# Optimization experiments

Hardware: AMD Instinct MI355X
Metric: run time of the kernel (lower is better)

## Reference

```python
import jax, jax.numpy as jnp
import numpy as np

N, E, EALL, C, R = 20000, 120000, 240000, 150, 1000
EH, RH, CH = 300, 100, 150


def _seg_softmax(e, idx, n):
    m = jax.ops.segment_max(e, idx, num_segments=n)
    ex = jnp.exp(e - m[idx])
    s = jax.ops.segment_sum(ex, idx, num_segments=n)
    return ex / s[idx]


def _l2norm(x):
    return x / jnp.clip(jnp.linalg.norm(x, axis=-1, keepdims=True), 1e-12, None)


def _highway(x1, x2, w, b):
    g = jax.nn.sigmoid(x1 @ w.T + b)
    return g * x2 + (1.0 - g) * x1


def _gcn(x, ei):
    n = x.shape[0]
    j, i = ei[0], ei[1]
    deg = jax.ops.segment_sum(jnp.ones(ei.shape[1], dtype=x.dtype), i, num_segments=n)
    dis = jnp.where(deg > 0, deg ** -0.5, 0.0)
    norm = dis[j] * dis[i]
    return jax.nn.relu(jax.ops.segment_sum(norm[:, None] * x[j], i, num_segments=n))


def _gat(x, ei, ai, aj):
    n = x.shape[0]
    j, i = ei[0], ei[1]
    e = (x @ ai)[i] + (x @ aj)[j]
    alpha = _seg_softmax(jax.nn.leaky_relu(e), i, n)
    return jax.nn.relu(jax.ops.segment_sum(alpha[:, None] * x[j], i, num_segments=n))


def _gat_e(x_e, im, io, rel, triple_num, r_emb, class_index, cls_ent,
           ac, ar, wh, wt, hww, hwb, main_is_head):
    n = x_e.shape[0]
    e_cnt = im.shape[0]
    c = cls_ent.shape[0]
    x_h = jax.nn.relu(x_e @ wh.T)
    x_t = jax.nn.relu(x_e @ wt.T)
    if main_is_head:
        x_m, x_o = x_h, x_t
        v1m, v2m, v3m = ac[0], ac[1], ac[2]
        v1o, v2o, v3o = ac[4], ac[5], ac[6]
    else:
        x_m, x_o = x_t, x_h
        v1m, v2m, v3m = ac[4], ac[5], ac[6]
        v1o, v2o, v3o = ac[0], ac[1], ac[2]
    v4, acv = ac[3], ac[7]
    e1 = 0.5 * ((x_m @ v1m)[im] + (x_o @ v1o)[io]) + (r_emb @ ar[0])[rel]
    alpha = _seg_softmax(jax.nn.leaky_relu(e1), triple_num, e_cnt)
    x_edge = _l2norm(x_m[im] * alpha[:, None])  # [E, c_hidden]
    e_r = 0.5 * ((r_emb @ ar[1])[rel] + 0.5 * ((x_edge @ v3m) + (x_o @ v3o)[io]))
    e = (x_o @ v2o)[io] + e_r + (x_edge @ v2m)
    beta = _seg_softmax(jax.nn.leaky_relu(e), class_index, c)
    # literal to source: the edge-level tensor is re-indexed by node ids in spmm
    x_class = jax.ops.segment_sum(beta[:, None] * x_edge[im], class_index, num_segments=c)
    e_c = (x_class @ acv) + (x_o @ v4)[cls_ent]
    gama = _seg_softmax(jax.nn.leaky_relu(e_c), cls_ent, n)
    out = jax.ops.segment_sum(gama[:, None] * x_class, cls_ent, num_segments=n)
    return _highway(x_o, out, hww, hwb)


def _forward(x_e, r_emb_table, hw1_w, hw1_b, hw2_w, hw2_b,
             h2r_ac, h2r_ar, h2r_wh, h2r_wt, h2r_hw_w, h2r_hw_b,
             et_ac, et_ar, et_wh, et_wt, et_hw_w, et_hw_b,
             gat_ai, gat_aj,
             edge_index, rel, edge_index_all, triple_num,
             class_index_head, head_class, class_index_tail, tail_class):
    r_emb = _l2norm(r_emb_table)
    x = _highway(x_e, _gcn(x_e, edge_index_all), hw1_w, hw1_b)
    x = _highway(x, _gcn(x, edge_index_all), hw2_w, hw2_b)
    eh, et = edge_index[0], edge_index[1]
    x_e_h = _gat_e(x, et, eh, rel, triple_num, r_emb, class_index_head, head_class,
                   h2r_ac, h2r_ar, h2r_wh, h2r_wt, h2r_hw_w, h2r_hw_b, False)
    x_e_t = _gat_e(x, eh, et, rel, triple_num, r_emb, class_index_tail, tail_class,
                   et_ac, et_ar, et_wh, et_wt, et_hw_w, et_hw_b, True)
    x1 = jnp.concatenate([x, x_e_h, x_e_t], axis=1)  # [N, 600]
    return jnp.concatenate([x, _gat(x1, edge_index_all, gat_ai, gat_aj)], axis=1)  # [N, 900]


def setup_inputs() -> dict:
    key = jax.random.key(0)
    ks = jax.random.split(key, 32)
    w = lambda k, shape: (jax.random.normal(k, shape, dtype=jnp.float32) * 0.05)
    return {
        'x_e': jax.random.normal(ks[0], (N, EH), dtype=jnp.float32),
        'edge_index': jax.random.randint(ks[1], (2, E), 0, N),
        'rel': jax.random.randint(ks[2], (E,), 0, R),
        'edge_index_all': jax.random.randint(ks[3], (2, EALL), 0, N),
        'triple_num': jax.random.randint(ks[4], (E,), 0, N),
        'class_index_head': jax.random.randint(ks[5], (E,), 0, C),
        'head_class': jax.random.randint(ks[6], (C,), 0, N),
        'class_index_tail': jax.random.randint(ks[7], (E,), 0, C),
        'tail_class': jax.random.randint(ks[8], (C,), 0, N),
        'r_emb_table': jax.random.normal(ks[9], (R, RH), dtype=jnp.float32),
        'hw1_w': w(ks[10], (EH, EH)), 'hw1_b': jnp.zeros((EH,), jnp.float32),
        'hw2_w': w(ks[11], (EH, EH)), 'hw2_b': jnp.zeros((EH,), jnp.float32),
        'h2r_ac': w(ks[12], (8, CH)), 'h2r_ar': w(ks[13], (2, RH)),
        'h2r_wh': w(ks[14], (CH, EH)), 'h2r_wt': w(ks[15], (CH, EH)),
        'h2r_hw_w': w(ks[16], (CH, CH)), 'h2r_hw_b': jnp.zeros((CH,), jnp.float32),
        'et_ac': w(ks[17], (8, CH)), 'et_ar': w(ks[18], (2, RH)),
        'et_wh': w(ks[19], (CH, EH)), 'et_wt': w(ks[20], (CH, EH)),
        'et_hw_w': w(ks[21], (CH, CH)), 'et_hw_b': jnp.zeros((CH,), jnp.float32),
        'gat_ai': w(ks[22], (2 * EH,)), 'gat_aj': w(ks[23], (2 * EH,)),
    }


def reference(x_e, edge_index, rel, edge_index_all, triple_num,
              class_index_head, head_class, class_index_tail, tail_class,
              r_emb_table, hw1_w, hw1_b, hw2_w, hw2_b,
              h2r_ac, h2r_ar, h2r_wh, h2r_wt, h2r_hw_w, h2r_hw_b,
              et_ac, et_ar, et_wh, et_wt, et_hw_w, et_hw_b,
              gat_ai, gat_aj):
    return _forward(x_e, r_emb_table, hw1_w, hw1_b, hw2_w, hw2_b,
                    h2r_ac, h2r_ar, h2r_wh, h2r_wt, h2r_hw_w, h2r_hw_b,
                    et_ac, et_ar, et_wh, et_wt, et_hw_w, et_hw_b,
                    gat_ai, gat_aj,
                    edge_index, rel, edge_index_all, triple_num,
                    class_index_head, head_class, class_index_tail, tail_class)
```

## Files before the change

kernel.cpp:

```cpp
#include <hip/hip_runtime.h>
#include <math.h>

#define Nn 20000
#define Ee 120000
#define EALLe 240000
#define Cc 150
#define Rr 1000
#define EHd 300
#define RHd 100
#define CHd 150
#define CB 128
#define XSPL 16

static inline int cdiv_h(int a, int b){ return (a + b - 1) / b; }

typedef __attribute__((ext_vector_type(8))) short short8;
typedef __attribute__((ext_vector_type(4))) float f32x4;

__device__ __forceinline__ float lrelu01(float x){ return x > 0.f ? x : 0.01f * x; }

__device__ __forceinline__ unsigned short f2b(float f){
  unsigned int u = __float_as_uint(f);
  unsigned int r = (u + 0x7FFFu + ((u >> 16) & 1u)) >> 16;
  return (unsigned short)r;
}
__device__ __forceinline__ float b2f(unsigned short u){
  return __uint_as_float(((unsigned int)u) << 16);
}
__device__ __forceinline__ float b2f_lo(unsigned int u){
  return __uint_as_float(u << 16);
}
__device__ __forceinline__ float b2f_hi(unsigned int u){
  return __uint_as_float(u & 0xFFFF0000u);
}

template<int Kq>
__device__ __forceinline__ void wredsumN(float* v){
#pragma unroll
  for (int m = 32; m >= 1; m >>= 1){
#pragma unroll
    for (int k = 0; k < Kq; k++) v[k] += __shfl_xor(v[k], m, 64);
  }
}

__global__ __launch_bounds__(64) void k_f2b(const float* __restrict__ src, int ncols,
    int ldsrc, unsigned short* __restrict__ dst, int ldp){
  int r = blockIdx.x, t = threadIdx.x;
  for (int c = t; c < ldp; c += 64)
    dst[(size_t)r * ldp + c] = (c < ncols) ? f2b(src[(size_t)r * ldsrc + c]) : (unsigned short)0;
}

__global__ __launch_bounds__(64) void k_f2bxo(const float* __restrict__ proj,
    unsigned short* __restrict__ xob){
  int r = blockIdx.x, g = blockIdx.y, t = threadIdx.x;
  const float* src = proj + (size_t)r * 600 + (g ? 450 : 0);
  unsigned short* dst = xob + (size_t)g * Nn * 160 + (size_t)r * 160;
  for (int c = t; c < 160; c += 64)
    dst[c] = (c < 150) ? f2b(src[c]) : (unsigned short)0;
}

__global__ __launch_bounds__(64) void k_rnorm(const float* __restrict__ rt,
    const float* __restrict__ arh, const float* __restrict__ are,
    float* __restrict__ ra1h, float* __restrict__ ra1e){
  int r = blockIdx.x, lane = threadIdx.x;
  bool m1 = (lane + 64 < RHd);
  float v0 = rt[r * RHd + lane];
  float v1 = m1 ? rt[r * RHd + lane + 64] : 0.f;
  float s[3];
  s[0] = v0 * v0 + v1 * v1;
  s[1] = v0 * arh[RHd + lane] + (m1 ? v1 * arh[RHd + lane + 64] : 0.f);
  s[2] = v0 * are[RHd + lane] + (m1 ? v1 * are[RHd + lane + 64] : 0.f);
  wredsumN<3>(s);
  float inv = 0.5f / fmaxf(sqrtf(s[0]), 1e-12f);
  if (!lane){
    ra1h[r] = s[1] * inv;
    ra1e[r] = s[2] * inv;
  }
}

__global__ void k_count(const int* __restrict__ dst, int* __restrict__ degi){
  int e = blockIdx.x * blockDim.x + threadIdx.x;
  if (e < EALLe) atomicAdd(&degi[dst[e]], 1);
}

__global__ void k_dis(const int* __restrict__ degi, float* __restrict__ dis){
  int n = blockIdx.x * blockDim.x + threadIdx.x;
  if (n < Nn) dis[n] = degi[n] > 0 ? rsqrtf((float)degi[n]) : 0.f;
}

__global__ __launch_bounds__(1024) void k_scan(const int* __restrict__ degi,
    int* __restrict__ ptr, int* __restrict__ cur){
  __shared__ int s[1024];
  int t = threadIdx.x;
  const int per = (Nn + 1023) / 1024;
  int b0 = t * per; if (b0 > Nn) b0 = Nn;
  int b1 = b0 + per; if (b1 > Nn) b1 = Nn;
  int sum = 0;
  for (int i = b0; i < b1; i++) sum += degi[i];
  s[t] = sum;
  __syncthreads();
  for (int off = 1; off < 1024; off <<= 1){
    int v = (t >= off) ? s[t - off] : 0;
    __syncthreads();
    s[t] += v;
    __syncthreads();
  }
  int run = (t > 0) ? s[t - 1] : 0;
  for (int i = b0; i < b1; i++){
    ptr[i] = run; cur[i] = run; run += degi[i];
  }
  if (t == 1023) ptr[Nn] = s[1023];
}

__global__ void k_scatter(const int* __restrict__ src, const int* __restrict__ dst,
    int* __restrict__ cur, int* __restrict__ csr_src){
  int e = blockIdx.x * blockDim.x + threadIdx.x;
  if (e >= EALLe) return;
  int pos = atomicAdd(&cur[dst[e]], 1);
  csr_src[pos] = src[e];
}

__global__ __launch_bounds__(64) void k_gcnb(const unsigned short* __restrict__ x, int ldx,
    const int* __restrict__ ptr, const int* __restrict__ src,
    const float* __restrict__ dis, float* __restrict__ out){
  int i = blockIdx.x, lane = threadIdx.x;
  int p0 = ptr[i], p1 = ptr[i + 1];
  float di = dis[i];
  float a0 = 0.f, a1 = 0.f, a2 = 0.f, a3 = 0.f, a4 = 0.f;
  for (int k = p0; k < p1; k++){
    int j = src[k];
    float w = di * dis[j];
    const unsigned short* xr = x + (size_t)j * ldx;
    a0 += w * b2f(xr[lane]);
    a1 += w * b2f(xr[lane + 64]);
    a2 += w * b2f(xr[lane + 128]);
    a3 += w * b2f(xr[lane + 192]);
    if (lane < EHd - 256) a4 += w * b2f(xr[lane + 256]);
  }
  float* orow = out + (size_t)i * EHd;
  orow[lane] = fmaxf(a0, 0.f);
  orow[lane + 64] = fmaxf(a1, 0.f);
  orow[lane + 128] = fmaxf(a2, 0.f);
  orow[lane + 192] = fmaxf(a3, 0.f);
  if (lane < EHd - 256) orow[lane + 256] = fmaxf(a4, 0.f);
}

__global__ __launch_bounds__(256) void k_gat3(const float* __restrict__ x1,
    const unsigned short* __restrict__ x1b,
    const int* __restrict__ ptr, const int* __restrict__ src,
    const float* __restrict__ s1, const float* __restrict__ s2,
    float* __restrict__ dout){
  __shared__ float wl[128];
  __shared__ int jl[128];
  int i = blockIdx.x, t = threadIdx.x;
  float* orow = dout + (size_t)i * 900;
  const float* xi = x1 + (size_t)i * 600;
  if (t < 75) ((f32x4*)orow)[t] = ((const f32x4*)xi)[t];
  int p0 = ptr[i], p1 = ptr[i + 1];
  if (p0 == p1){
    for (int f = t; f < 600; f += 256) orow[300 + f] = 0.f;
    return;
  }
  float s1i = s1[i];
  bool m2 = t < 44;
  float a0 = 0.f, a1 = 0.f, c0 = 0.f, c1 = 0.f, den = 0.f;
  for (int base = p0; base < p1; base += 128){
    int k = base + t;
    if (t < 128 && k < p1){
      int j = src[k];
      jl[t] = j;
      wl[t] = expf(lrelu01(s1i + s2[j]));
    }
    __syncthreads();
    int lim = p1 - base; if (lim > 128) lim = 128;
    for (int q = 0; q < lim; q++){
      float w = wl[q];
      den += w;
      const unsigned short* xj = x1b + (size_t)jl[q] * 600;
      unsigned int u = *(const unsigned int*)&xj[2 * t];
      a0 += w * b2f_lo(u);
      a1 += w * b2f_hi(u);
      if (m2){
        unsigned int v = *(const unsigned int*)&xj[512 + 2 * t];
        c0 += w * b2f_lo(v);
        c1 += w * b2f_hi(v);
      }
    }
    __syncthreads();
  }
  float invd = 1.f / den;
  orow[300 + 2 * t] = fmaxf(a0 * invd, 0.f);
  orow[300 + 2 * t + 1] = fmaxf(a1 * invd, 0.f);
  if (m2){
    orow[300 + 512 + 2 * t] = fmaxf(c0 * invd, 0.f);
    orow[300 + 512 + 2 * t + 1] = fmaxf(c1 * invd, 0.f);
  }
}

template<int EPI, int MIR>
__global__ __launch_bounds__(256) void k_gemmb(
    const unsigned short* __restrict__ Xb, int ldxb, int nrows,
    const unsigned short* __restrict__ Wb, int Kp, int M,
    const float* __restrict__ bias,
    const float* __restrict__ X2, int ldx2,
    const float* __restrict__ Xf, int ldxf,
    float* __restrict__ out, int ldo,
    unsigned short* __restrict__ mir, int ldmir){
  __shared__ unsigned short Xs[64][40];
  __shared__ unsigned short Ws[64][40];
  int t = threadIdx.x;
  int wv = t >> 6, lane = t & 63;
  int c0 = blockIdx.x * 64, r0 = blockIdx.y * 64;
  int srow = t >> 2, skoff = (t & 3) * 8;
  int gxr = r0 + srow, gwr = c0 + srow;
  f32x4 acc[4] = {};
  for (int k0 = 0; k0 < Kp; k0 += 32){
    short8 xv = {0,0,0,0,0,0,0,0};
    short8 wv8 = {0,0,0,0,0,0,0,0};
    if (gxr < nrows) xv = *(const short8*)&Xb[(size_t)gxr * ldxb + k0 + skoff];
    if (gwr < M)     wv8 = *(const short8*)&Wb[(size_t)gwr * Kp + k0 + skoff];
    __syncthreads();
    *(short8*)&Xs[srow][skoff] = xv;
    *(short8*)&Ws[srow][skoff] = wv8;
    __syncthreads();
    int arow = wv * 16 + (lane & 15);
    int kk = (lane >> 4) * 8;
    short8 af = *(const short8*)&Xs[arow][kk];
#pragma unroll
    for (int j = 0; j < 4; j++){
      short8 bf = *(const short8*)&Ws[j * 16 + (lane & 15)][kk];
      acc[j] = __builtin_amdgcn_mfma_f32_16x16x32_bf16(af, bf, acc[j], 0, 0, 0);
    }
  }
  int rbase = r0 + wv * 16 + (lane >> 4) * 4;
  int cbase = c0 + (lane & 15);
#pragma unroll
  for (int j = 0; j < 4; j++){
    int c = cbase + j * 16;
    if (c >= M) continue;
#pragma unroll
    for (int r = 0; r < 4; r++){
      int row = rbase + r;
      if (row >= nrows) continue;
      float v = acc[j][r];
      float o;
      if (EPI == 0){
        o = fmaxf(v, 0.f);
      } else {
        float g = 1.f / (1.f + expf(-(v + bias[c])));
        o = g * X2[(size_t)row * ldx2 + c] + (1.f - g) * Xf[(size_t)row * ldxf + c];
      }
      out[(size_t)row * ldo + c] = o;
      if (MIR) mir[(size_t)row * ldmir + c] = f2b(o);
    }
  }
}

__global__ __launch_bounds__(256) void k_hwgemm(
    const unsigned short* __restrict__ xob,
    const unsigned short* __restrict__ hwwbA, const unsigned short* __restrict__ hwwbB,
    const float* __restrict__ hwbA, const float* __restrict__ hwbB,
    const float* __restrict__ outb, const float* __restrict__ proj,
    float* __restrict__ x1, unsigned short* __restrict__ x1b){
  __shared__ unsigned short Xs[64][40];
  __shared__ unsigned short Ws[64][40];
  int g = blockIdx.z;
  const unsigned short* Xb = xob + (size_t)g * Nn * 160;
  const unsigned short* Wb = g ? hwwbB : hwwbA;
  const float* bias = g ? hwbB : hwbA;
  const float* X2 = outb + (size_t)g * Nn * CHd;
  const float* Xf = proj + (g ? 450 : 0);
  float* outp = x1 + (g ? 450 : 300);
  unsigned short* mir = x1b + (g ? 450 : 300);
  int t = threadIdx.x;
  int wv = t >> 6, lane = t & 63;
  int c0 = blockIdx.x * 64, r0 = blockIdx.y * 64;
  int srow = t >> 2, skoff = (t & 3) * 8;
  int gxr = r0 + srow, gwr = c0 + srow;
  f32x4 acc[4] = {};
  for (int k0 = 0; k0 < 160; k0 += 32){
    short8 xv = {0,0,0,0,0,0,0,0};
    short8 wv8 = {0,0,0,0,0,0,0,0};
    if (gxr < Nn) xv = *(const short8*)&Xb[(size_t)gxr * 160 + k0 + skoff];
    if (gwr < 150) wv8 = *(const short8*)&Wb[(size_t)gwr * 160 + k0 + skoff];
    __syncthreads();
    *(short8*)&Xs[srow][skoff] = xv;
    *(short8*)&Ws[srow][skoff] = wv8;
    __syncthreads();
    int arow = wv * 16 + (lane & 15);
    int kk = (lane >> 4) * 8;
    short8 af = *(const short8*)&Xs[arow][kk];
#pragma unroll
    for (int j = 0; j < 4; j++){
      short8 bf = *(const short8*)&Ws[j * 16 + (lane & 15)][kk];
      acc[j] = __builtin_amdgcn_mfma_f32_16x16x32_bf16(af, bf, acc[j], 0, 0, 0);
    }
  }
  int rbase = r0 + wv * 16 + (lane >> 4) * 4;
  int cbase = c0 + (lane & 15);
#pragma unroll
  for (int j = 0; j < 4; j++){
    int c = cbase + j * 16;
    if (c >= 150) continue;
#pragma unroll
    for (int r = 0; r < 4; r++){
      int row = rbase + r;
      if (row >= Nn) continue;
      float v = acc[j][r];
      float gg = 1.f / (1.f + expf(-(v + bias[c])));
      float o = gg * X2[(size_t)row * CHd + c] + (1.f - gg) * Xf[(size_t)row * 600 + c];
      outp[(size_t)row * 600 + c] = o;
      mir[(size_t)row * 600 + c] = f2b(o);
    }
  }
}

__global__ __launch_bounds__(64) void k_ndots2b(const float* __restrict__ proj,
    const float* __restrict__ h2r_ac, const float* __restrict__ et_ac,
    unsigned short* __restrict__ xnb, float* __restrict__ pm,
    float* __restrict__ po, float* __restrict__ nv4){
  int n = blockIdx.x, g = blockIdx.y, lane = threadIdx.x;
  const float* ac = g ? et_ac : h2r_ac;
  const float* xm = proj + (g ? 300 : 150);
  const float* xo = proj + (g ? 450 : 0);
  const float* v2m = ac + (g ? 1 : 5) * CHd;
  const float* v2o = ac + (g ? 5 : 1) * CHd;
  const float* v3m = ac + (g ? 2 : 6) * CHd;
  const float* v3o = ac + (g ? 6 : 2) * CHd;
  const float* v4  = ac + 3 * CHd;
  bool m2 = lane < (CHd - 128);
  const float* mr = xm + (size_t)n * 600;
  const float* orw = xo + (size_t)n * 600;
  float m0 = mr[lane], m1 = mr[lane + 64], mv2 = m2 ? mr[lane + 128] : 0.f;
  float o0 = orw[lane], o1 = orw[lane + 64], o2 = m2 ? orw[lane + 128] : 0.f;
  float s[4];
  s[0] = m0 * m0 + m1 * m1 + mv2 * mv2;
  s[1] = o0 * v2o[lane] + o1 * v2o[lane + 64] + (m2 ? o2 * v2o[lane + 128] : 0.f);
  s[2] = o0 * v3o[lane] + o1 * v3o[lane + 64] + (m2 ? o2 * v3o[lane + 128] : 0.f);
  s[3] = o0 * v4[lane]  + o1 * v4[lane + 64]  + (m2 ? o2 * v4[lane + 128]  : 0.f);
  wredsumN<4>(s);
  float inv = 1.f / fmaxf(sqrtf(s[0]), 1e-12f);
  float n0 = m0 * inv, n1 = m1 * inv, n2 = mv2 * inv;
  unsigned short* xr = xnb + (size_t)g * Nn * 152 + (size_t)n * 152;
  xr[lane] = f2b(n0); xr[lane + 64] = f2b(n1);
  if (m2) xr[lane + 128] = f2b(n2);
  float d[2];
  d[0] = n0 * v2m[lane] + n1 * v2m[lane + 64] + (m2 ? n2 * v2m[lane + 128] : 0.f);
  d[1] = n0 * v3m[lane] + n1 * v3m[lane + 64] + (m2 ? n2 * v3m[lane + 128] : 0.f);
  wredsumN<2>(d);
  if (!lane){
    pm[g * Nn + n] = d[0] + 0.25f * d[1];
    po[g * Nn + n] = s[1] + 0.25f * s[2];
    nv4[g * Nn + n] = s[3];
  }
}

__global__ __launch_bounds__(256) void k_e2sumb(const int* __restrict__ ei,
    const int* __restrict__ rel, const int* __restrict__ cih, const int* __restrict__ cit,
    const float* __restrict__ pm, const float* __restrict__ po,
    const float* __restrict__ ra1h, const float* __restrict__ ra1e,
    float* __restrict__ es2, float* __restrict__ csum_p, int* __restrict__ ccnt_p){
  __shared__ float ls[Cc];
  __shared__ int lc[Cc];
  int t = threadIdx.x, g = blockIdx.y;
  const int* im = ei + (g ? 0 : Ee);
  const int* io = ei + (g ? Ee : 0);
  const int* ci = g ? cit : cih;
  const float* ra1 = g ? ra1e : ra1h;
  const float* pmg = pm + g * Nn;
  const float* pog = po + g * Nn;
  float* es2g = es2 + (size_t)g * Ee;
  float* csg = csum_p + g * Cc * 16;
  int* ccg = ccnt_p + g * Cc * 16;
  for (int c = t; c < Cc; c += 256){ ls[c] = 0.f; lc[c] = 0; }
  __syncthreads();
  for (int e = blockIdx.x * 256 + t; e < Ee; e += gridDim.x * 256){
    float v = lrelu01(pog[io[e]] + pmg[im[e]] + ra1[rel[e]]);
    float s = expf(v);
    es2g[e] = s;
    int c = ci[e];
    atomicAdd(&ls[c], s);
    atomicAdd(&lc[c], 1);
  }
  __syncthreads();
  for (int c = t; c < Cc; c += 256){
    if (lc[c]){
      atomicAdd(&csg[c * 16], ls[c]);
      atomicAdd(&ccg[c * 16], lc[c]);
    }
  }
}

__global__ __launch_bounds__(256) void k_cscanb(const int* __restrict__ ccnt_p,
    int* __restrict__ cstart, int* __restrict__ ccur_p){
  __shared__ int s[Cc + 1];
  int t = threadIdx.x, g = blockIdx.x;
  const int* ccg = ccnt_p + g * Cc * 16;
  int* csg = cstart + g * (Cc + 1);
  int* cug = ccur_p + g * Cc * 16;
  if (t == 0){
    int run = 0;
    for (int c = 0; c < Cc; c++){ s[c] = run; run += ccg[c * 16]; }
    s[Cc] = run;
  }
  __syncthreads();
  if (t <= Cc) csg[t] = s[t];
  if (t < Cc) cug[t * 16] = s[t];
}

__global__ __launch_bounds__(256) void k_cscatterb(const int* __restrict__ ei,
    const int* __restrict__ cih, const int* __restrict__ cit,
    const float* __restrict__ es2,
    int* __restrict__ ccur_p, int* __restrict__ crows, float* __restrict__ cw){
  __shared__ int lcnt[Cc];
  __shared__ int lbase[Cc];
  int t = threadIdx.x, g = blockIdx.y;
  const int* im = ei + (g ? 0 : Ee);
  const int* ci = g ? cit : cih;
  const float* es2g = es2 + (size_t)g * Ee;
  int* cug = ccur_p + g * Cc * 16;
  int* crg = crows + (size_t)g * Ee;
  float* cwg = cw + (size_t)g * Ee;
  int epb = (Ee + gridDim.x - 1) / gridDim.x;
  int e0 = blockIdx.x * epb, e1 = e0 + epb; if (e1 > Ee) e1 = Ee;
  for (int c = t; c < Cc; c += 256) lcnt[c] = 0;
  __syncthreads();
  int myr[4], myc[4], mye[4]; int cnt = 0;
  for (int e = e0 + t; e < e1; e += 256){
    int c = ci[e];
    myr[cnt] = atomicAdd(&lcnt[c], 1);
    myc[cnt] = c; mye[cnt] = e; cnt++;
  }
  __syncthreads();
  for (int c = t; c < Cc; c += 256)
    lbase[c] = lcnt[c] ? atomicAdd(&cug[c * 16], lcnt[c]) : 0;
  __syncthreads();
  for (int q = 0; q < cnt; q++){
    int pos = lbase[myc[q]] + myr[q];
    int e = mye[q];
    crg[pos] = im[im[e]];
    cwg[pos] = es2g[e];
  }
}

__global__ __launch_bounds__(192) void k_xclassBb(
    const int* __restrict__ cstart, const int* __restrict__ crows,
    const float* __restrict__ cw, const float* __restrict__ csum_p,
    const unsigned short* __restrict__ xnb, float* __restrict__ x_class){
  int g = blockIdx.y;
  int c = blockIdx.x / XSPL, sp = blockIdx.x % XSPL;
  int t = threadIdx.x;
  const int* csg = cstart + g * (Cc + 1);
  const int* crg = crows + (size_t)g * Ee;
  const float* cwg = cw + (size_t)g * Ee;
  const unsigned short* xng = xnb + (size_t)g * Nn * 152;
  float* xcg = x_class + g * Cc * CHd;
  int p0 = csg[c], p1 = csg[c + 1];
  int len = p1 - p0;
  if (len <= 0) return;
  int chunk = (len + XSPL - 1) / XSPL;
  int q0 = p0 + sp * chunk;
  int q1 = q0 + chunk; if (q1 > p1) q1 = p1;
  if (q0 >= q1) return;
  bool act = t < CHd;
  float inv = 1.f / csum_p[g * Cc * 16 + c * 16];
  float acc = 0.f;
  int k = q0;
  for (; k + 4 <= q1; k += 4){
    int r0 = crg[k], r1 = crg[k + 1], r2 = crg[k + 2], r3 = crg[k + 3];
    float w0 = cwg[k] * inv, w1 = cwg[k + 1] * inv, w2 = cwg[k + 2] * inv, w3 = cwg[k + 3] * inv;
    if (act){
      acc += w0 * b2f(xng[(size_t)r0 * 152 + t]) + w1 * b2f(xng[(size_t)r1 * 152 + t])
           + w2 * b2f(xng[(size_t)r2 * 152 + t]) + w3 * b2f(xng[(size_t)r3 * 152 + t]);
    }
  }
  for (; k < q1; k++){
    if (act) acc += cwg[k] * inv * b2f(xng[(size_t)crg[k] * 152 + t]);
  }
  if (act) atomicAdd(&xcg[c * CHd + t], acc);
}

__global__ __launch_bounds__(256) void k_classfinalb(
    const float* __restrict__ x_class,
    const float* __restrict__ h2r_ac, const float* __restrict__ et_ac,
    const float* __restrict__ nv4,
    const int* __restrict__ hcls, const int* __restrict__ tcls,
    float* __restrict__ outb){
  __shared__ float v[Cc];
  __shared__ float gm[Cc];
  __shared__ int ce[Cc];
  int t = threadIdx.x, g = blockIdx.x;
  const float* xcg = x_class + g * Cc * CHd;
  const float* acv = (g ? et_ac : h2r_ac) + 7 * CHd;
  const float* nvg = nv4 + g * Nn;
  const int* cls_ent = g ? tcls : hcls;
  float* obg = outb + (size_t)g * Nn * CHd;
  if (t < Cc){
    ce[t] = cls_ent[t];
    float dot = 0.f;
    for (int f = 0; f < CHd; f++) dot += xcg[t * CHd + f] * acv[f];
    v[t] = lrelu01(dot + nvg[ce[t]]);
  }
  __syncthreads();
  if (t < Cc){
    int sgm = ce[t];
    float m = -3.0e38f;
    for (int c2 = 0; c2 < Cc; c2++) if (ce[c2] == sgm) m = fmaxf(m, v[c2]);
    float sum = 0.f;
    for (int c2 = 0; c2 < Cc; c2++) if (ce[c2] == sgm) sum += expf(v[c2] - m);
    gm[t] = expf(v[t] - m) / sum;
  }
  __syncthreads();
  for (int idx = t; idx < Cc * CHd; idx += 256){
    int c = idx / CHd, f = idx - c * CHd;
    atomicAdd(&obg[(size_t)ce[c] * CHd + f], gm[c] * xcg[c * CHd + f]);
  }
}

__global__ __launch_bounds__(64) void k_s12(const unsigned short* __restrict__ x1b,
    const float* __restrict__ ai, const float* __restrict__ aj,
    float* __restrict__ s1, float* __restrict__ s2){
  int n = blockIdx.x, lane = threadIdx.x;
  const unsigned short* xr = x1b + (size_t)n * 600;
  float sa = 0.f, sb = 0.f;
#pragma unroll
  for (int u = 0; u < 10; u++){
    int f = lane + u * 64;
    if (f < 600){
      float x = b2f(xr[f]);
      sa += x * ai[f];
      sb += x * aj[f];
    }
  }
  float s[2] = { sa, sb };
  wredsumN<2>(s);
  if (!lane){ s1[n] = s[0]; s2[n] = s[1]; }
}

extern "C" void kernel_launch(void* const* d_in, const int* in_sizes, int n_in,
                              void* d_out, int out_size, void* d_ws, size_t ws_size,
                              hipStream_t stream) {
  const float* x_e    = (const float*)d_in[0];
  const int*   ei     = (const int*)d_in[1];
  const int*   rel    = (const int*)d_in[2];
  const int*   eall   = (const int*)d_in[3];
  const int*   cih    = (const int*)d_in[5];
  const int*   hcls   = (const int*)d_in[6];
  const int*   cit    = (const int*)d_in[7];
  const int*   tcls   = (const int*)d_in[8];
  const float* remb   = (const float*)d_in[9];
  const float* hw1w   = (const float*)d_in[10];
  const float* hw1b   = (const float*)d_in[11];
  const float* hw2w   = (const float*)d_in[12];
  const float* hw2b   = (const float*)d_in[13];
  const float* h2r_ac = (const float*)d_in[14];
  const float* h2r_ar = (const float*)d_in[15];
  const float* h2r_wh = (const float*)d_in[16];
  const float* h2r_wt = (const float*)d_in[17];
  const float* h2r_hww= (const float*)d_in[18];
  const float* h2r_hwb= (const float*)d_in[19];
  const float* et_ac  = (const float*)d_in[20];
  const float* et_ar  = (const float*)d_in[21];
  const float* et_wh  = (const float*)d_in[22];
  const float* et_wt  = (const float*)d_in[23];
  const float* et_hww = (const float*)d_in[24];
  const float* et_hwb = (const float*)d_in[25];
  const float* gai    = (const float*)d_in[26];
  const float* gaj    = (const float*)d_in[27];
  float* out = (float*)d_out;

  char* wsp = (char*)d_ws;
  auto alloc = [&](size_t nbytes) -> void* {
    void* p = (void*)wsp;
    wsp += (nbytes + 255) & ~(size_t)255;
    return p;
  };
  float* ra1h = (float*)alloc(Rr * 4);
  float* ra1e = (float*)alloc(Rr * 4);
  float* dis  = (float*)alloc(Nn * 4);
  int* degi    = (int*)alloc(Nn * 4);
  int* csr_ptr = (int*)alloc((Nn + 1) * 4);
  int* csr_cur = (int*)alloc(Nn * 4);
  int* csr_src = (int*)alloc((size_t)EALLe * 4);
  float* x1  = (float*)alloc((size_t)Nn * 600 * 4);
  float* es2 = (float*)alloc((size_t)2 * Ee * 4);
  float* pm  = (float*)alloc(2 * Nn * 4);
  float* po  = (float*)alloc(2 * Nn * 4);
  float* nv4 = (float*)alloc(2 * Nn * 4);
  float* csum_p = (float*)alloc(2 * Cc * 16 * 4);
  int*   ccnt_p = (int*)alloc(2 * Cc * 16 * 4);
  float* x_class = (float*)alloc(2 * Cc * CHd * 4);
  size_t zregion = (size_t)((char*)x_class + ((2 * Cc * CHd * 4 + 255) & ~255)) - (size_t)(char*)csum_p;
  int*   ccur_p = (int*)alloc(2 * Cc * 16 * 4);
  int*   cstart = (int*)alloc(2 * (Cc + 1) * 4);
  int*   crows  = (int*)alloc((size_t)2 * Ee * 4);
  float* cw     = (float*)alloc((size_t)2 * Ee * 4);
  float* s1v = (float*)alloc(Nn * 4);
  float* s2v = (float*)alloc(Nn * 4);
  unsigned short* arenaA = (unsigned short*)alloc((size_t)Nn * 320 * 2);
  unsigned short* arenaB = (unsigned short*)alloc((size_t)Nn * 320 * 2);
  unsigned short* x1b    = (unsigned short*)alloc(((size_t)Nn * 600 + 64) * 2);
  unsigned short* w1b    = (unsigned short*)alloc((size_t)300 * 320 * 2);
  unsigned short* w2b    = (unsigned short*)alloc((size_t)300 * 320 * 2);
  unsigned short* wcatb  = (unsigned short*)alloc((size_t)600 * 320 * 2);
  unsigned short* hwwbA  = (unsigned short*)alloc((size_t)150 * 160 * 2);
  unsigned short* hwwbB  = (unsigned short*)alloc((size_t)150 * 160 * 2);
  unsigned short* xob = arenaA;
  unsigned short* xnb = arenaB;

  float* h1   = out;
  float* gbuf = out + (size_t)Nn * EHd;
  float* proj = out;
  float* outb = out + (size_t)Nn * 600;

  hipMemsetAsync(degi, 0, Nn * 4, stream);
  hipMemsetAsync(csum_p, 0, zregion, stream);
  hipMemsetAsync(outb, 0, (size_t)2 * Nn * CHd * 4, stream);
  k_rnorm<<<Rr, 64, 0, stream>>>(remb, h2r_ar, et_ar, ra1h, ra1e);
  k_count<<<cdiv_h(EALLe, 256), 256, 0, stream>>>(eall + EALLe, degi);
  k_dis<<<cdiv_h(Nn, 256), 256, 0, stream>>>(degi, dis);
  k_scan<<<1, 1024, 0, stream>>>(degi, csr_ptr, csr_cur);
  k_scatter<<<cdiv_h(EALLe, 256), 256, 0, stream>>>(eall, eall + EALLe, csr_cur, csr_src);
  k_f2b<<<300, 64, 0, stream>>>(hw1w, 300, 300, w1b, 320);
  k_f2b<<<300, 64, 0, stream>>>(hw2w, 300, 300, w2b, 320);
  k_f2b<<<150, 64, 0, stream>>>(h2r_wh, 300, 300, wcatb + (size_t)0   * 320, 320);
  k_f2b<<<150, 64, 0, stream>>>(h2r_wt, 300, 300, wcatb + (size_t)150 * 320, 320);
  k_f2b<<<150, 64, 0, stream>>>(et_wh,  300, 300, wcatb + (size_t)300 * 320, 320);
  k_f2b<<<150, 64, 0, stream>>>(et_wt,  300, 300, wcatb + (size_t)450 * 320, 320);
  k_f2b<<<150, 64, 0, stream>>>(h2r_hww, 150, 150, hwwbA, 160);
  k_f2b<<<150, 64, 0, stream>>>(et_hww,  150, 150, hwwbB, 160);
  k_f2b<<<Nn, 64, 0, stream>>>(x_e, 300, 300, arenaA, 320);

  k_gcnb<<<Nn, 64, 0, stream>>>(arenaA, 320, csr_ptr, csr_src, dis, gbuf);
  k_gemmb<1,1><<<dim3(5, cdiv_h(Nn, 64)), 256, 0, stream>>>(
      arenaA, 320, Nn, w1b, 320, 300, hw1b, gbuf, 300, x_e, 300, h1, 300, arenaB, 320);
  k_gcnb<<<Nn, 64, 0, stream>>>(arenaB, 320, csr_ptr, csr_src, dis, gbuf);
  k_gemmb<1,1><<<dim3(5, cdiv_h(Nn, 64)), 256, 0, stream>>>(
      arenaB, 320, Nn, w2b, 320, 300, hw2b, gbuf, 300, h1, 300, x1, 600, x1b, 600);

  k_gemmb<0,0><<<dim3(10, cdiv_h(Nn, 64)), 256, 0, stream>>>(
      x1b, 600, Nn, wcatb, 320, 600, nullptr, nullptr, 0, nullptr, 0, proj, 600,
      nullptr, 0);

  k_f2bxo<<<dim3(Nn, 2), 64, 0, stream>>>(proj, xob);
  k_ndots2b<<<dim3(Nn, 2), 64, 0, stream>>>(proj, h2r_ac, et_ac, xnb, pm, po, nv4);
  k_e2sumb<<<dim3(CB, 2), 256, 0, stream>>>(ei, rel, cih, cit, pm, po, ra1h, ra1e,
                                            es2, csum_p, ccnt_p);
  k_cscanb<<<2, 256, 0, stream>>>(ccnt_p, cstart, ccur_p);
  k_cscatterb<<<dim3(CB, 2), 256, 0, stream>>>(ei, cih, cit, es2, ccur_p, crows, cw);
  k_xclassBb<<<dim3(Cc * XSPL, 2), 192, 0, stream>>>(cstart, crows, cw, csum_p,
                                                     xnb, x_class);
  k_classfinalb<<<2, 256, 0, stream>>>(x_class, h2r_ac, et_ac, nv4, hcls, tcls, outb);
  k_hwgemm<<<dim3(3, cdiv_h(Nn, 64), 2), 256, 0, stream>>>(
      xob, hwwbA, hwwbB, h2r_hwb, et_hwb, outb, proj, x1, x1b);

  k_s12<<<Nn, 64, 0, stream>>>(x1b, gai, gaj, s1v, s2v);
  k_gat3<<<Nn, 256, 0, stream>>>(x1, x1b, csr_ptr, csr_src, s1v, s2v, out);
}
```

Measured before the change: 549.2 us.

## Batch weight conversions, fuse small kernels, vectorize bf16 loads in GCN and s12

```diff
diff --git a/kernel.cpp b/kernel.cpp
--- a/kernel.cpp
+++ b/kernel.cpp
@@ -50,13 +50,22 @@
     dst[(size_t)r * ldp + c] = (c < ncols) ? f2b(src[(size_t)r * ldsrc + c]) : (unsigned short)0;
 }
 
-__global__ __launch_bounds__(64) void k_f2bxo(const float* __restrict__ proj,
-    unsigned short* __restrict__ xob){
-  int r = blockIdx.x, g = blockIdx.y, t = threadIdx.x;
-  const float* src = proj + (size_t)r * 600 + (g ? 450 : 0);
-  unsigned short* dst = xob + (size_t)g * Nn * 160 + (size_t)r * 160;
-  for (int c = t; c < 160; c += 64)
-    dst[c] = (c < 150) ? f2b(src[c]) : (unsigned short)0;
+struct Cvt8 {
+  const float* s[8];
+  unsigned short* d[8];
+  int nc[8]; int lds[8]; int ldp[8]; int r0[9];
+};
+__global__ __launch_bounds__(64) void k_f2ball(Cvt8 c){
+  int b = blockIdx.x, t = threadIdx.x;
+  int idx = 0;
+#pragma unroll
+  for (int q = 1; q < 8; q++) if (b >= c.r0[q]) idx = q;
+  int r = b - c.r0[idx];
+  const float* src = c.s[idx] + (size_t)r * c.lds[idx];
+  unsigned short* dst = c.d[idx] + (size_t)r * c.ldp[idx];
+  int nc = c.nc[idx], ldp = c.ldp[idx];
+  for (int col = t; col < ldp; col += 64)
+    dst[col] = (col < nc) ? f2b(src[col]) : (unsigned short)0;
 }
 
 __global__ __launch_bounds__(64) void k_rnorm(const float* __restrict__ rt,
@@ -83,13 +92,8 @@
   if (e < EALLe) atomicAdd(&degi[dst[e]], 1);
 }
 
-__global__ void k_dis(const int* __restrict__ degi, float* __restrict__ dis){
-  int n = blockIdx.x * blockDim.x + threadIdx.x;
-  if (n < Nn) dis[n] = degi[n] > 0 ? rsqrtf((float)degi[n]) : 0.f;
-}
-
 __global__ __launch_bounds__(1024) void k_scan(const int* __restrict__ degi,
-    int* __restrict__ ptr, int* __restrict__ cur){
+    int* __restrict__ ptr, int* __restrict__ cur, float* __restrict__ dis){
   __shared__ int s[1024];
   int t = threadIdx.x;
   const int per = (Nn + 1023) / 1024;
@@ -107,7 +111,9 @@
   }
   int run = (t > 0) ? s[t - 1] : 0;
   for (int i = b0; i < b1; i++){
-    ptr[i] = run; cur[i] = run; run += degi[i];
+    int dg = degi[i];
+    ptr[i] = run; cur[i] = run; run += dg;
+    dis[i] = dg > 0 ? rsqrtf((float)dg) : 0.f;
   }
   if (t == 1023) ptr[Nn] = s[1023];
 }
@@ -120,29 +126,36 @@
   csr_src[pos] = src[e];
 }
 
-__global__ __launch_bounds__(64) void k_gcnb(const unsigned short* __restrict__ x, int ldx,
+__global__ __launch_bounds__(64) void k_gcnb(const unsigned short* __restrict__ x,
     const int* __restrict__ ptr, const int* __restrict__ src,
     const float* __restrict__ dis, float* __restrict__ out){
   int i = blockIdx.x, lane = threadIdx.x;
   int p0 = ptr[i], p1 = ptr[i + 1];
   float di = dis[i];
-  float a0 = 0.f, a1 = 0.f, a2 = 0.f, a3 = 0.f, a4 = 0.f;
+  bool m2 = lane < 22;
+  float a0 = 0.f, a1 = 0.f, b0 = 0.f, b1 = 0.f, c0 = 0.f, c1 = 0.f;
   for (int k = p0; k < p1; k++){
     int j = src[k];
     float w = di * dis[j];
-    const unsigned short* xr = x + (size_t)j * ldx;
-    a0 += w * b2f(xr[lane]);
-    a1 += w * b2f(xr[lane + 64]);
-    a2 += w * b2f(xr[lane + 128]);
-    a3 += w * b2f(xr[lane + 192]);
-    if (lane < EHd - 256) a4 += w * b2f(xr[lane + 256]);
+    const unsigned int* xr = (const unsigned int*)(x + (size_t)j * 320);
+    unsigned int u0 = xr[lane];
+    unsigned int u1 = xr[lane + 64];
+    a0 += w * b2f_lo(u0); a1 += w * b2f_hi(u0);
+    b0 += w * b2f_lo(u1); b1 += w * b2f_hi(u1);
+    if (m2){
+      unsigned int u2 = xr[lane + 128];
+      c0 += w * b2f_lo(u2); c1 += w * b2f_hi(u2);
+    }
   }
   float* orow = out + (size_t)i * EHd;
-  orow[lane] = fmaxf(a0, 0.f);
-  orow[lane + 64] = fmaxf(a1, 0.f);
-  orow[lane + 128] = fmaxf(a2, 0.f);
-  orow[lane + 192] = fmaxf(a3, 0.f);
-  if (lane < EHd - 256) orow[lane + 256] = fmaxf(a4, 0.f);
+  orow[2 * lane]       = fmaxf(a0, 0.f);
+  orow[2 * lane + 1]   = fmaxf(a1, 0.f);
+  orow[128 + 2 * lane]     = fmaxf(b0, 0.f);
+  orow[128 + 2 * lane + 1] = fmaxf(b1, 0.f);
+  if (m2){
+    orow[256 + 2 * lane]     = fmaxf(c0, 0.f);
+    orow[256 + 2 * lane + 1] = fmaxf(c1, 0.f);
+  }
 }
 
 __global__ __launch_bounds__(256) void k_gat3(const float* __restrict__ x1,
@@ -317,6 +330,7 @@
 
 __global__ __launch_bounds__(64) void k_ndots2b(const float* __restrict__ proj,
     const float* __restrict__ h2r_ac, const float* __restrict__ et_ac,
+    unsigned short* __restrict__ xob,
     unsigned short* __restrict__ xnb, float* __restrict__ pm,
     float* __restrict__ po, float* __restrict__ nv4){
   int n = blockIdx.x, g = blockIdx.y, lane = threadIdx.x;
@@ -333,6 +347,11 @@
   const float* orw = xo + (size_t)n * 600;
   float m0 = mr[lane], m1 = mr[lane + 64], mv2 = m2 ? mr[lane + 128] : 0.f;
   float o0 = orw[lane], o1 = orw[lane + 64], o2 = m2 ? orw[lane + 128] : 0.f;
+  unsigned short* xod = xob + (size_t)g * Nn * 160 + (size_t)n * 160;
+  xod[lane] = f2b(o0);
+  xod[lane + 64] = f2b(o1);
+  if (m2) xod[lane + 128] = f2b(o2);
+  if (lane < 10) xod[150 + lane] = 0;
   float s[4];
   s[0] = m0 * m0 + m1 * m1 + mv2 * mv2;
   s[1] = o0 * v2o[lane] + o1 * v2o[lane + 64] + (m2 ? o2 * v2o[lane + 128] : 0.f);
@@ -521,15 +540,16 @@
     const float* __restrict__ ai, const float* __restrict__ aj,
     float* __restrict__ s1, float* __restrict__ s2){
   int n = blockIdx.x, lane = threadIdx.x;
-  const unsigned short* xr = x1b + (size_t)n * 600;
+  const unsigned int* xr = (const unsigned int*)(x1b + (size_t)n * 600);
   float sa = 0.f, sb = 0.f;
 #pragma unroll
-  for (int u = 0; u < 10; u++){
-    int f = lane + u * 64;
-    if (f < 600){
-      float x = b2f(xr[f]);
-      sa += x * ai[f];
-      sb += x * aj[f];
+  for (int u = 0; u < 5; u++){
+    int d = lane + u * 64;
+    if (d < 300){
+      unsigned int w = xr[d];
+      float xlo = b2f_lo(w), xhi = b2f_hi(w);
+      sa += xlo * ai[2 * d] + xhi * ai[2 * d + 1];
+      sb += xlo * aj[2 * d] + xhi * aj[2 * d + 1];
     }
   }
   float s[2] = { sa, sb };
@@ -618,23 +638,28 @@
   hipMemsetAsync(outb, 0, (size_t)2 * Nn * CHd * 4, stream);
   k_rnorm<<<Rr, 64, 0, stream>>>(remb, h2r_ar, et_ar, ra1h, ra1e);
   k_count<<<cdiv_h(EALLe, 256), 256, 0, stream>>>(eall + EALLe, degi);
-  k_dis<<<cdiv_h(Nn, 256), 256, 0, stream>>>(degi, dis);
-  k_scan<<<1, 1024, 0, stream>>>(degi, csr_ptr, csr_cur);
+  k_scan<<<1, 1024, 0, stream>>>(degi, csr_ptr, csr_cur, dis);
   k_scatter<<<cdiv_h(EALLe, 256), 256, 0, stream>>>(eall, eall + EALLe, csr_cur, csr_src);
-  k_f2b<<<300, 64, 0, stream>>>(hw1w, 300, 300, w1b, 320);
-  k_f2b<<<300, 64, 0, stream>>>(hw2w, 300, 300, w2b, 320);
-  k_f2b<<<150, 64, 0, stream>>>(h2r_wh, 300, 300, wcatb + (size_t)0   * 320, 320);
-  k_f2b<<<150, 64, 0, stream>>>(h2r_wt, 300, 300, wcatb + (size_t)150 * 320, 320);
-  k_f2b<<<150, 64, 0, stream>>>(et_wh,  300, 300, wcatb + (size_t)300 * 320, 320);
-  k_f2b<<<150, 64, 0, stream>>>(et_wt,  300, 300, wcatb + (size_t)450 * 320, 320);
-  k_f2b<<<150, 64, 0, stream>>>(h2r_hww, 150, 150, hwwbA, 160);
-  k_f2b<<<150, 64, 0, stream>>>(et_hww,  150, 150, hwwbB, 160);
+  {
+    Cvt8 cv;
+    cv.s[0] = hw1w;    cv.d[0] = w1b;                         cv.nc[0] = 300; cv.lds[0] = 300; cv.ldp[0] = 320;
+    cv.s[1] = hw2w;    cv.d[1] = w2b;                         cv.nc[1] = 300; cv.lds[1] = 300; cv.ldp[1] = 320;
+    cv.s[2] = h2r_wh;  cv.d[2] = wcatb + (size_t)0   * 320;   cv.nc[2] = 300; cv.lds[2] = 300; cv.ldp[2] = 320;
+    cv.s[3] = h2r_wt;  cv.d[3] = wcatb + (size_t)150 * 320;   cv.nc[3] = 300; cv.lds[3] = 300; cv.ldp[3] = 320;
+    cv.s[4] = et_wh;   cv.d[4] = wcatb + (size_t)300 * 320;   cv.nc[4] = 300; cv.lds[4] = 300; cv.ldp[4] = 320;
+    cv.s[5] = et_wt;   cv.d[5] = wcatb + (size_t)450 * 320;   cv.nc[5] = 300; cv.lds[5] = 300; cv.ldp[5] = 320;
+    cv.s[6] = h2r_hww; cv.d[6] = hwwbA;                       cv.nc[6] = 150; cv.lds[6] = 150; cv.ldp[6] = 160;
+    cv.s[7] = et_hww;  cv.d[7] = hwwbB;                       cv.nc[7] = 150; cv.lds[7] = 150; cv.ldp[7] = 160;
+    cv.r0[0] = 0;    cv.r0[1] = 300;  cv.r0[2] = 600;  cv.r0[3] = 750;
+    cv.r0[4] = 900;  cv.r0[5] = 1050; cv.r0[6] = 1200; cv.r0[7] = 1350; cv.r0[8] = 1500;
+    k_f2ball<<<1500, 64, 0, stream>>>(cv);
+  }
   k_f2b<<<Nn, 64, 0, stream>>>(x_e, 300, 300, arenaA, 320);
 
-  k_gcnb<<<Nn, 64, 0, stream>>>(arenaA, 320, csr_ptr, csr_src, dis, gbuf);
+  k_gcnb<<<Nn, 64, 0, stream>>>(arenaA, csr_ptr, csr_src, dis, gbuf);
   k_gemmb<1,1><<<dim3(5, cdiv_h(Nn, 64)), 256, 0, stream>>>(
       arenaA, 320, Nn, w1b, 320, 300, hw1b, gbuf, 300, x_e, 300, h1, 300, arenaB, 320);
-  k_gcnb<<<Nn, 64, 0, stream>>>(arenaB, 320, csr_ptr, csr_src, dis, gbuf);
+  k_gcnb<<<Nn, 64, 0, stream>>>(arenaB, csr_ptr, csr_src, dis, gbuf);
   k_gemmb<1,1><<<dim3(5, cdiv_h(Nn, 64)), 256, 0, stream>>>(
       arenaB, 320, Nn, w2b, 320, 300, hw2b, gbuf, 300, h1, 300, x1, 600, x1b, 600);
 
@@ -642,8 +667,7 @@
       x1b, 600, Nn, wcatb, 320, 600, nullptr, nullptr, 0, nullptr, 0, proj, 600,
       nullptr, 0);
 
-  k_f2bxo<<<dim3(Nn, 2), 64, 0, stream>>>(proj, xob);
-  k_ndots2b<<<dim3(Nn, 2), 64, 0, stream>>>(proj, h2r_ac, et_ac, xnb, pm, po, nv4);
+  k_ndots2b<<<dim3(Nn, 2), 64, 0, stream>>>(proj, h2r_ac, et_ac, xob, xnb, pm, po, nv4);
   k_e2sumb<<<dim3(CB, 2), 256, 0, stream>>>(ei, rel, cih, cit, pm, po, ra1h, ra1e,
                                             es2, csum_p, ccnt_p);
   k_cscanb<<<2, 256, 0, stream>>>(ccnt_p, cstart, ccur_p);
```

Measured after the change: 525.7 us. -4.3%, faster.
